# Performance work log

Measured on AMD Instinct MI355X. Metric: run time of the kernel, lower is better.

The kernel has to match this reference:

```python
import jax, jax.numpy as jnp
import numpy as np

N, E_SC, E_BB = 50000, 600000, 100000
D, ED, REMB, NRES, SBF = 128, 128, 32, 21, 16
PI = 3.14159


def ln(x, g, b):
    m = jnp.mean(x, -1, keepdims=True)
    v = jnp.mean((x - m) ** 2, -1, keepdims=True)
    return (x - m) * jax.lax.rsqrt(v + 1e-5) * g + b


def gcn(x, W, b, src, dst, w):
    # GCNConv: symmetric normalization with unit self-loops and edge weights w.
    n = x.shape[0]
    xw = x @ W
    deg = jax.ops.segment_sum(w, dst, num_segments=n) + 1.0  # +1 self-loop
    dis = jax.lax.rsqrt(jnp.maximum(deg, 1e-6))  # clamp: hat_e.mean can be negative
    norm = dis[src] * w * dis[dst]
    agg = jax.ops.segment_sum(norm[:, None] * xw[src], dst, num_segments=n)
    return agg + (dis * dis)[:, None] * xw + b


def core(V_com, SBF_chi, X_c_alpha, V_c_beta, SBF_phi, SBF_psi, d_sidechain_com, d_min,
         old_chi, old_phi, old_psi, old_cbeta_coords, old_calpha_coords,
         res_table, sc_ln_g, sc_ln_b, sc_W, sc_b, bb_ln_g, bb_ln_b, bb_W, bb_b,
         e_ln_g, e_ln_b, eW1, eb1, eW2, eb2, euW, eub, gW, gb, bgW, bgb,
         iW1, ib1, iW2, ib2, aW, ab, baW, bab, cW, cb, xW, xb,
         residue_idx_i, residue_idx_j, edge_index_sc, edge_index_bb):
    hat_h = ln(jnp.concatenate([V_com, SBF_chi], -1), sc_ln_g, sc_ln_b) @ sc_W + sc_b
    h = ln(jnp.concatenate([X_c_alpha, V_c_beta, SBF_phi, SBF_psi], -1), bb_ln_g, bb_ln_b) @ bb_W + bb_b
    pair = jnp.concatenate([res_table[residue_idx_i], res_table[residue_idx_j]], -1)
    e_in = jnp.concatenate([d_sidechain_com[:, None], d_min[:, None], pair], -1)
    hat_e = jax.nn.relu(ln(e_in, e_ln_g, e_ln_b) @ eW1 + eb1) @ eW2 + eb2
    src, dst = edge_index_sc[0], edge_index_sc[1]
    for _ in range(3):  # num_sidechain_layers
        w = hat_e.mean(-1)
        hat_h = hat_h + jax.nn.relu(gcn(hat_h, gW, gb, src, dst, w))
        hat_e = hat_e + jnp.concatenate([hat_h[src], hat_h[dst]], -1) @ euW + eub
    bsrc, bdst = edge_index_bb[0], edge_index_bb[1]
    ebb = jnp.ones(bsrc.shape[0], hat_h.dtype)
    for _ in range(2):
        m = jax.nn.relu(jnp.concatenate([h, hat_h], -1) @ iW1 + ib1) @ iW2 + ib2
        h = h + jax.nn.relu(gcn(h, bgW, bgb, bsrc, bdst, ebb)) + m
    sc_act = jax.nn.relu(hat_h)
    bb_act = jax.nn.relu(h)
    wrap = lambda a: (a + PI) % (2.0 * PI) - PI
    dchi = (sc_act @ aW + ab)[:, 0]
    chi_new = wrap(old_chi + dchi[None, :])  # [4, N]
    dphi = (bb_act @ baW + bab)[:, 0]
    phi_new = wrap(old_phi + dphi)
    psi_new = wrap(old_psi + dphi)  # same bb_angle_head applied twice in source
    V_cbeta_new = old_cbeta_coords + sc_act @ cW + cb
    X_calpha_new = old_calpha_coords + bb_act @ xW + xb
    return chi_new, phi_new, psi_new, V_cbeta_new, X_calpha_new


def setup_inputs() -> dict:
    key = jax.random.key(0)
    ks = jax.random.split(key, 40)
    rn = lambda i, s: jax.random.normal(ks[i], s, jnp.float32)
    p = lambda i, s: rn(i, s) * 0.05
    return dict(
        V_com=rn(0, (N, 3)), SBF_chi=rn(1, (N, SBF)), X_c_alpha=rn(2, (N, 3)),
        V_c_beta=rn(3, (N, 3)), SBF_phi=rn(4, (N, SBF)), SBF_psi=rn(5, (N, SBF)),
        d_sidechain_com=jax.random.uniform(ks[6], (E_SC,), jnp.float32),
        d_min=jax.random.uniform(ks[7], (E_SC,), jnp.float32),
        old_chi=rn(8, (4, N)), old_phi=rn(9, (N,)), old_psi=rn(10, (N,)),
        old_cbeta_coords=rn(11, (N, 3)), old_calpha_coords=rn(12, (N, 3)),
        res_table=p(13, (NRES, REMB)),
        sc_ln_g=jnp.ones(3 + SBF), sc_ln_b=jnp.zeros(3 + SBF), sc_W=p(14, (3 + SBF, D)), sc_b=jnp.zeros(D),
        bb_ln_g=jnp.ones(6 + 2 * SBF), bb_ln_b=jnp.zeros(6 + 2 * SBF), bb_W=p(15, (6 + 2 * SBF, D)), bb_b=jnp.zeros(D),
        e_ln_g=jnp.ones(2 + 2 * REMB), e_ln_b=jnp.zeros(2 + 2 * REMB),
        eW1=p(16, (2 + 2 * REMB, ED)), eb1=jnp.zeros(ED), eW2=p(17, (ED, ED)), eb2=jnp.zeros(ED),
        euW=p(18, (2 * D, ED)), eub=jnp.zeros(ED),
        gW=p(19, (D, D)), gb=jnp.zeros(D), bgW=p(20, (D, D)), bgb=jnp.zeros(D),
        iW1=p(21, (2 * D, D)), ib1=jnp.zeros(D), iW2=p(22, (D, D)), ib2=jnp.zeros(D),
        aW=p(23, (D, 1)), ab=jnp.zeros(1), baW=p(24, (D, 1)), bab=jnp.zeros(1),
        cW=p(25, (D, 3)), cb=jnp.zeros(3), xW=p(26, (D, 3)), xb=jnp.zeros(3),
        residue_idx_i=jax.random.randint(ks[27], (E_SC,), 0, NRES),
        residue_idx_j=jax.random.randint(ks[28], (E_SC,), 0, NRES),
        edge_index_sc=jax.random.randint(ks[29], (2, E_SC), 0, N),
        edge_index_bb=jax.random.randint(ks[30], (2, E_BB), 0, N),
    )


def reference(V_com, SBF_chi, X_c_alpha, V_c_beta, SBF_phi, SBF_psi, d_sidechain_com, d_min,
              old_chi, old_phi, old_psi, old_cbeta_coords, old_calpha_coords,
              res_table, sc_ln_g, sc_ln_b, sc_W, sc_b, bb_ln_g, bb_ln_b, bb_W, bb_b,
              e_ln_g, e_ln_b, eW1, eb1, eW2, eb2, euW, eub, gW, gb, bgW, bgb,
              iW1, ib1, iW2, ib2, aW, ab, baW, bab, cW, cb, xW, xb,
              residue_idx_i, residue_idx_j, edge_index_sc, edge_index_bb):
    return core(V_com, SBF_chi, X_c_alpha, V_c_beta, SBF_phi, SBF_psi, d_sidechain_com, d_min,
                old_chi, old_phi, old_psi, old_cbeta_coords, old_calpha_coords,
                res_table, sc_ln_g, sc_ln_b, sc_W, sc_b, bb_ln_g, bb_ln_b, bb_W, bb_b,
                e_ln_g, e_ln_b, eW1, eb1, eW2, eb2, euW, eub, gW, gb, bgW, bgb,
                iW1, ib1, iW2, ib2, aW, ab, baW, bab, cW, cb, xW, xb,
                residue_idx_i, residue_idx_j, edge_index_sc, edge_index_bb)
```

## Files before the change

### kernel.cpp

```cpp
#include <hip/hip_runtime.h>
#include <stdint.h>

#define DEVI __device__ __forceinline__

constexpr int N_   = 50000;
constexpr int ESC  = 600000;
constexpr int EBB  = 100000;
constexpr int NRES = 21;
constexpr float PI_F = 3.14159f;

constexpr int RCH = 2048;
constexpr int RBS = (ESC + RCH - 1)/RCH;
constexpr int RBB = (EBB + RCH - 1)/RCH;

typedef __attribute__((ext_vector_type(8))) short short8v;
typedef __attribute__((ext_vector_type(4))) float f32x4;

DEVI float bf2f(unsigned short u){ return __uint_as_float(((unsigned)u)<<16); }
DEVI unsigned short f2bf(float f){
  unsigned x = __float_as_uint(f);
  unsigned r = (x + 0x7FFFu + ((x>>16)&1u))>>16;
  return (unsigned short)r;
}
DEVI float ldin(const void* p, long i, int f32){
  return f32 ? ((const float*)p)[i] : bf2f(((const unsigned short*)p)[i]);
}
DEVI void stout(void* p, long i, float v, int f32){
  if(f32) ((float*)p)[i]=v; else ((unsigned short*)p)[i]=f2bf(v);
}
DEVI float wrapf(float a){
  float t = a + PI_F;
  const float TP = 2.f*PI_F;
  t -= floorf(t/TP)*TP;
  return t - PI_F;
}

constexpr int OW_SC_LN_G=0;
constexpr int OW_SC_LN_B=OW_SC_LN_G+19;
constexpr int OW_SC_W  = OW_SC_LN_B+19;
constexpr int OW_SC_B  = OW_SC_W+19*128;
constexpr int OW_BB_LN_G=OW_SC_B+128;
constexpr int OW_BB_LN_B=OW_BB_LN_G+38;
constexpr int OW_BB_W = OW_BB_LN_B+38;
constexpr int OW_BB_B = OW_BB_W+38*128;
constexpr int OW_E_LN_G=OW_BB_B+128;
constexpr int OW_E_LN_B=OW_E_LN_G+66;
constexpr int OW_EW1 = OW_E_LN_B+66;
constexpr int OW_EB1 = OW_EW1+66*128;
constexpr int OW_GW  = OW_EB1+128;
constexpr int OW_GB  = OW_GW+128*128;
constexpr int OW_BGW = OW_GB+128;
constexpr int OW_BGB = OW_BGW+128*128;
constexpr int OW_IW1 = OW_BGB+128;
constexpr int OW_IB1 = OW_IW1+256*128;
constexpr int OW_IW2 = OW_IB1+128;
constexpr int OW_IB2 = OW_IW2+128*128;
constexpr int OW_AW  = OW_IB2+128;
constexpr int OW_AB  = OW_AW+128;
constexpr int OW_BAW = OW_AB+1;
constexpr int OW_BAB = OW_BAW+128;
constexpr int OW_CW  = OW_BAB+1;
constexpr int OW_CB  = OW_CW+128*3;
constexpr int OW_XW  = OW_CB+3;
constexpr int OW_XB  = OW_XW+128*3;
constexpr int OW_RES = OW_XB+3;
constexpr int OW_TOT = OW_RES+21*32;

__global__ void k_detect(const void* vcom, int* flag){
  const unsigned short* u = (const unsigned short*)vcom;
  int insane=0;
  for(int i=0;i<64;i+=2){
    float f = bf2f(u[i]);
    float a = fabsf(f);
    if(!(a<1e5f) || (a!=0.0f && a<1e-5f)) insane++;
  }
  *flag = (insane>=8)?1:0;
}

struct CvtArgs { const void* src[29]; };

__global__ void k_cvtw(CvtArgs a, const int* flag, float* w){
  static constexpr int offs[30] = {
    OW_SC_LN_G,OW_SC_LN_B,OW_SC_W,OW_SC_B,OW_BB_LN_G,OW_BB_LN_B,OW_BB_W,OW_BB_B,
    OW_E_LN_G,OW_E_LN_B,OW_EW1,OW_EB1,OW_GW,OW_GB,OW_BGW,OW_BGB,OW_IW1,OW_IB1,
    OW_IW2,OW_IB2,OW_AW,OW_AB,OW_BAW,OW_BAB,OW_CW,OW_CB,OW_XW,OW_XB,OW_RES,OW_TOT};
  int f32=*flag;
  for(int t=blockIdx.x*blockDim.x+threadIdx.x; t<OW_TOT; t+=gridDim.x*blockDim.x){
    int s=0;
    while(t>=offs[s+1]) s++;
    w[t]=ldin(a.src[s], t-offs[s], f32);
  }
}

DEVI void wprep_pad(const float* W, int Kreal, unsigned short* hi, unsigned short* lo, int idx){
  int lane=idx&63, nt=(idx>>6)&7, kt=idx>>9;
  int n = nt*16 + (lane&15);
  int kbase = kt*32 + (lane>>4)*8;
  #pragma unroll
  for(int i=0;i<8;i++){
    int k=kbase+i;
    float v = (k<Kreal) ? W[(long)k*128 + n] : 0.f;
    unsigned short h = f2bf(v);
    hi[(long)idx*8+i]=h;
    if(lo){ float r = v - bf2f(h); lo[(long)idx*8+i]=f2bf(r); }
  }
}

constexpr int PB_WP = 46;
constexpr int PB_PV = PB_WP+1;
constexpr int PB_PP = PB_PV+441;
constexpr int PB_LN = PB_PP + (2*N_+3)/4;

__global__ void k_prep(const float* w, const int* flag,
    unsigned short* g_hi, unsigned short* g_lo,
    unsigned short* bg_hi,
    unsigned short* i2_hi,
    unsigned short* i1_hi,
    unsigned short* sc_hi, unsigned short* sc_lo,
    unsigned short* bb_hi, unsigned short* bb_lo,
    const void* eW2, const void* eb2, const void* euW, const void* eub,
    float* dv, float* dv4, float* P, float* sp, float* qp,
    const void* vcom, const void* sbfchi,
    const void* xca, const void* vcb, const void* sphi, const void* spsi,
    float* xn_sc, float* xn_bb){
  __shared__ float pv[64];
  int b=blockIdx.x;
  if(b<PB_WP){
    int idx=b*256+threadIdx.x;
    if(idx<2048)       wprep_pad(w+OW_GW,  128, g_hi,  g_lo,  idx);
    else if(idx<4096)  wprep_pad(w+OW_BGW, 128, bg_hi, nullptr, idx-2048);
    else if(idx<6144)  wprep_pad(w+OW_IW2, 128, i2_hi, nullptr, idx-4096);
    else if(idx<10240) wprep_pad(w+OW_IW1, 256, i1_hi, nullptr, idx-6144);
    else if(idx<10752) wprep_pad(w+OW_SC_W, 19, sc_hi, sc_lo, idx-10240);
    else if(idx<11776) wprep_pad(w+OW_BB_W, 38, bb_hi, bb_lo, idx-10752);
  } else if(b<PB_PV){
    int j=threadIdx.x; int f32=*flag;
    if(j<128){
      const float* g=w+OW_E_LN_G; const float* bb=w+OW_E_LN_B; const float* W1=w+OW_EW1;
      float A=g[0]*W1[j], C=g[1]*W1[128+j];
      float G=0,B=0;
      for(int i=0;i<66;i++){ float wij=W1[i*128+j]; G+=g[i]*wij; B+=bb[i]*wij; }
      B += w[OW_EB1+j];
      float v2=0; for(int k=0;k<128;k++) v2+=ldin(eW2,(long)j*128+k,f32);
      float us=0,ud=0;
      for(int k=0;k<128;k++){ us+=ldin(euW,(long)j*128+k,f32); ud+=ldin(euW,(long)(128+j)*128+k,f32); }
      dv[640+j]=us*(1.f/128.f); dv[768+j]=ud*(1.f/128.f);
      int j4=j>>2, r=j&3;
      dv4[j4*20+0+r]=A; dv4[j4*20+4+r]=C; dv4[j4*20+8+r]=G; dv4[j4*20+12+r]=B;
      dv4[j4*20+16+r]=v2*(1.f/128.f);
      if(j==0){
        float s=0,t=0;
        for(int k=0;k<128;k++){ s+=ldin(eb2,k,f32); t+=ldin(eub,k,f32); }
        dv[896]=s*(1.f/128.f); dv[897]=t*(1.f/128.f);
        dv4[640]=s*(1.f/128.f);
      }
    }
  } else if(b<PB_PP){
    int c=b-PB_PV, j=threadIdx.x;
    const float* res=w+OW_RES;
    if(j<32) pv[j]=res[(c/NRES)*32+j];
    else if(j<64) pv[j]=res[(c%NRES)*32+(j-32)];
    __syncthreads();
    if(j<128){
      const float* g=w+OW_E_LN_G; const float* W1=w+OW_EW1;
      float s=0;
      for(int i=0;i<64;i++) s += pv[i]*g[2+i]*W1[(2+i)*128+j];
      P[c*128+j]=s;
      if(j==0){ float a=0,q=0; for(int i=0;i<64;i++){a+=pv[i]; q+=pv[i]*pv[i];} sp[c]=a; qp[c]=q; }
    }
  } else {
    int wv=threadIdx.x>>6, lane=threadIdx.x&63;
    long gw=(long)(b-PB_PP)*4+wv;
    int f32=*flag;
    if(gw<N_){
      int n=(int)gw;
      float x=0.f;
      if(lane<3) x=ldin(vcom,(long)n*3+lane,f32);
      else if(lane<19) x=ldin(sbfchi,(long)n*16+(lane-3),f32);
      float s=x, q=x*x;
      for(int m=1;m<64;m<<=1){ s+=__shfl_xor(s,m,64); q+=__shfl_xor(q,m,64); }
      float mean=s*(1.f/19.f);
      float istd=rsqrtf(fmaxf(q*(1.f/19.f)-mean*mean,0.f)+1e-5f);
      if(lane<32){
        float xn=(lane<19)? (x-mean)*istd*w[OW_SC_LN_G+lane]+w[OW_SC_LN_B+lane] : 0.f;
        xn_sc[(long)n*32+lane]=xn;
      }
    } else if(gw<2L*N_){
      int n=(int)(gw-N_);
      float x=0.f;
      if(lane<3) x=ldin(xca,(long)n*3+lane,f32);
      else if(lane<6) x=ldin(vcb,(long)n*3+(lane-3),f32);
      else if(lane<22) x=ldin(sphi,(long)n*16+(lane-6),f32);
      else if(lane<38) x=ldin(spsi,(long)n*16+(lane-22),f32);
      float s=x, q=x*x;
      for(int m=1;m<64;m<<=1){ s+=__shfl_xor(s,m,64); q+=__shfl_xor(q,m,64); }
      float mean=s*(1.f/38.f);
      float istd=rsqrtf(fmaxf(q*(1.f/38.f)-mean*mean,0.f)+1e-5f);
      float xn=(lane<38)? (x-mean)*istd*w[OW_BB_LN_G+lane]+w[OW_BB_LN_B+lane] : 0.f;
      xn_bb[(long)n*64+lane]=xn;
    }
  }
}

__global__ void k_rhist(const int* key_sc, const int* key_bb, int shift, int* hist){
  __shared__ int h[256];
  h[threadIdx.x]=0; __syncthreads();
  int g = blockIdx.x>=RBS;
  const int* key = g? key_bb : key_sc;
  int E = g? EBB : ESC;
  int b = g? blockIdx.x-RBS : blockIdx.x;
  int base=b*RCH;
  for(int r=0;r<RCH/256;r++){
    int idx=base+r*256+threadIdx.x;
    if(idx<E) atomicAdd(&h[(key[idx]>>shift)&255],1);
  }
  __syncthreads();
  hist[(long)blockIdx.x*256+threadIdx.x]=h[threadIdx.x];
}
__global__ void k_rscanA(int* hist, int* tot){
  __shared__ int sA[512], sB[512];
  int g = blockIdx.x>=256;
  int d = blockIdx.x&255;
  int NB = g? RBB : RBS;
  int* H = hist + (g? (long)RBS*256 : 0);
  int t=threadIdx.x;
  int i0=t, i1=t+256;
  int o0 = (i0<NB)? H[(long)i0*256+d] : 0;
  int o1 = (i1<NB)? H[(long)i1*256+d] : 0;
  sA[i0]=o0; sA[i1]=o1;
  __syncthreads();
  int* a=sA; int* b=sB;
  for(int off=1; off<512; off<<=1){
    b[i0] = a[i0] + ((i0>=off)? a[i0-off]:0);
    b[i1] = a[i1] + ((i1>=off)? a[i1-off]:0);
    __syncthreads();
    int* tmp=a; a=b; b=tmp;
  }
  if(i0<NB) H[(long)i0*256+d] = a[i0]-o0;
  if(i1<NB) H[(long)i1*256+d] = a[i1]-o1;
  if(t==255) tot[(g?256:0)+d] = a[511];
}
__global__ void k_rscanB(const int* tot, int* base){
  __shared__ int sA[256], sB[256];
  int t=threadIdx.x;
  for(int g=0;g<2;g++){
    int o=tot[g*256+t];
    sA[t]=o; __syncthreads();
    int* a=sA; int* b=sB;
    for(int off=1; off<256; off<<=1){
      b[t] = a[t] + ((t>=off)? a[t-off]:0);
      __syncthreads();
      int* tmp=a; a=b; b=tmp;
    }
    base[g*256+t] = a[t]-o;
    __syncthreads();
  }
}
__global__ void k_rscat(int shift, int first,
    const int* kin_sc, const int* srcv_sc, const int2* pin_sc,
    const int* kin_bb, const int* srcv_bb, const int2* pin_bb,
    const int* hist, const int* dbase,
    int* kout_sc, int2* pout_sc, int* kout_bb, int2* pout_bb){
  __shared__ int running[256];
  __shared__ int Hb[256];
  __shared__ int whist[4][256];
  __shared__ int pw[4][256];
  int tid=threadIdx.x, lane=tid&63, w=tid>>6;
  int g = blockIdx.x>=RBS;
  const int* kin  = g? kin_bb : kin_sc;
  const int* srcv = g? srcv_bb: srcv_sc;
  const int2* pin = g? pin_bb : pin_sc;
  int* kout  = g? kout_bb : kout_sc;
  int2* pout = g? pout_bb : pout_sc;
  int E = g? EBB : ESC;
  int b = g? blockIdx.x-RBS : blockIdx.x;
  running[tid]=0;
  Hb[tid]=hist[(long)blockIdx.x*256+tid] + dbase[(g?256:0)+tid];
  int base=b*RCH;
  for(int r=0;r<RCH/256;r++){
    __syncthreads();
    whist[0][tid]=0; whist[1][tid]=0; whist[2][tid]=0; whist[3][tid]=0;
    __syncthreads();
    int idx=base+r*256+tid;
    bool valid = idx<E;
    int key=0, digit=0; int2 pay; pay.x=0; pay.y=0;
    if(valid){
      key=kin[idx];
      digit=(key>>shift)&255;
      if(first){ pay.x=srcv[idx]; pay.y=idx; }
      else pay=pin[idx];
    }
    unsigned long long act=__ballot(valid);
    unsigned long long same=act;
    #pragma unroll
    for(int k=0;k<8;k++){
      unsigned long long m=__ballot(valid && ((digit>>k)&1));
      same &= ((digit>>k)&1)? m : ~m;
    }
    same &= act;
    unsigned long long below=(1ULL<<lane)-1ULL;
    int wrank=__popcll(same & below);
    if(valid && wrank==0) whist[w][digit]=__popcll(same);
    __syncthreads();
    int c0=whist[0][tid], c1=whist[1][tid], c2=whist[2][tid], c3=whist[3][tid];
    pw[0][tid]=0; pw[1][tid]=c0; pw[2][tid]=c0+c1; pw[3][tid]=c0+c1+c2;
    __syncthreads();
    if(valid){
      int pos=Hb[digit]+running[digit]+pw[w][digit]+wrank;
      kout[pos]=key; pout[pos]=pay;
    }
    __syncthreads();
    running[tid]+=c0+c1+c2+c3;
  }
}
__global__ void k_bounds(const int* dstS_sc, const int* dstS_bb, int* rp_sc, int* rp_bb){
  long i=(long)blockIdx.x*blockDim.x+threadIdx.x;
  if(i<=ESC){
    int cur = (i<ESC)? dstS_sc[i] : N_;
    int prev= (i>0)? dstS_sc[i-1] : -1;
    for(int d=prev+1; d<=cur; d++) rp_sc[d]=(int)i;
  } else if(i <= (long)ESC+1+EBB){
    long j=i-(ESC+1);
    int cur = (j<EBB)? dstS_bb[j] : N_;
    int prev= (j>0)? dstS_bb[j-1] : -1;
    for(int d=prev+1; d<=cur; d++) rp_bb[d]=(int)j;
  }
}
__global__ void k_degb(const int* rp, float* disb){
  int n=blockIdx.x*blockDim.x+threadIdx.x;
  if(n<N_) disb[n]=rsqrtf(1.f+(float)(rp[n+1]-rp[n]));
}

constexpr int WB4 = (ESC + 1023)/1024;
__global__ __launch_bounds__(256,4) void k_w0(const void* dsc, const void* dmin,
    const int* ri_, const int* rj_, const int* flag, const float* dv4,
    const float* P, const float* sp, const float* qp, float* we){
  long base=(long)blockIdx.x*1024+threadIdx.x;
  int f32=*flag;
  float d1[4],d2[4],istd[4],nmi[4],acc[4];
  int cc[4]; bool val[4];
  #pragma unroll
  for(int k=0;k<4;k++){
    long e=base+k*256;
    val[k]= e<ESC;
    long ee= val[k]? e : 0;
    d1[k]=ldin(dsc,ee,f32); d2[k]=ldin(dmin,ee,f32);
    int c=ri_[ee]*NRES+rj_[ee];
    cc[k]=c;
    float m=(d1[k]+d2[k]+sp[c])*(1.f/66.f);
    float ms=(d1[k]*d1[k]+d2[k]*d2[k]+qp[c])*(1.f/66.f);
    istd[k]=rsqrtf(fmaxf(ms-m*m,0.f)+1e-5f);
    nmi[k]=-m*istd[k];
    acc[k]=0.f;
  }
  #pragma unroll 2
  for(int j4=0;j4<32;j4++){
    const float4* q=(const float4*)&dv4[j4*20];
    float4 A4=q[0], C4=q[1], G4=q[2], B4=q[3], V4=q[4];
    #pragma unroll
    for(int k=0;k<4;k++){
      float4 P4=*(const float4*)&P[(long)cc[k]*128+j4*4];
      float t,hid;
      t=fmaf(d1[k],A4.x,fmaf(d2[k],C4.x,P4.x)); hid=fmaf(istd[k],t,fmaf(nmi[k],G4.x,B4.x)); acc[k]=fmaf(fmaxf(hid,0.f),V4.x,acc[k]);
      t=fmaf(d1[k],A4.y,fmaf(d2[k],C4.y,P4.y)); hid=fmaf(istd[k],t,fmaf(nmi[k],G4.y,B4.y)); acc[k]=fmaf(fmaxf(hid,0.f),V4.y,acc[k]);
      t=fmaf(d1[k],A4.z,fmaf(d2[k],C4.z,P4.z)); hid=fmaf(istd[k],t,fmaf(nmi[k],G4.z,B4.z)); acc[k]=fmaf(fmaxf(hid,0.f),V4.z,acc[k]);
      t=fmaf(d1[k],A4.w,fmaf(d2[k],C4.w,P4.w)); hid=fmaf(istd[k],t,fmaf(nmi[k],G4.w,B4.w)); acc[k]=fmaf(fmaxf(hid,0.f),V4.w,acc[k]);
    }
  }
  float e2=dv4[640];
  #pragma unroll
  for(int k=0;k<4;k++) if(val[k]) we[base+k*256]=acc[k]+e2;
}

__global__ void k_deg(const int* rp, const int2* se, const float* we_edge,
                      const float* an, const float* bn, const float* dv,
                      float* we_csr, float* dis, int layer){
  int n=blockIdx.x*blockDim.x+threadIdx.x;
  if(n>=N_) return;
  int e0=rp[n], e1=rp[n+1];
  float s=1.f;
  if(layer==0){
    for(int p=e0;p<e1;p++){ float ww=we_edge[se[p].y]; we_csr[p]=ww; s+=ww; }
  } else {
    float add_n = bn[n] + dv[897];
    for(int p=e0;p<e1;p++){
      float ww=we_csr[p] + an[se[p].x] + add_n;
      we_csr[p]=ww; s+=ww;
    }
  }
  dis[n]=rsqrtf(fmaxf(s,1e-6f));
}
__global__ void k_norm(const int2* se, const float* we_csr, const float* dis, float* wn){
  int p=blockIdx.x*blockDim.x+threadIdx.x;
  if(p<ESC) wn[p]=dis[se[p].x]*we_csr[p];
}

DEVI f32x4 MFMA(short8v a, short8v b, f32x4 c){
  return __builtin_amdgcn_mfma_f32_16x16x32_bf16(a,b,c,0,0,0);
}
DEVI void cvt8(float4 a0, float4 a1, short8v& hi, short8v& lo){
  float av[8]={a0.x,a0.y,a0.z,a0.w,a1.x,a1.y,a1.z,a1.w};
  union{short8v v; unsigned short u[8];} H,L;
  #pragma unroll
  for(int i=0;i<8;i++){
    unsigned short h=f2bf(av[i]);
    float r=av[i]-bf2f(h);
    H.u[i]=h; L.u[i]=f2bf(r);
  }
  hi=H.v; lo=L.v;
}
DEVI short8v cvt8hi(float4 a0, float4 a1){
  union{short8v v; unsigned short u[8];} H;
  H.u[0]=f2bf(a0.x); H.u[1]=f2bf(a0.y); H.u[2]=f2bf(a0.z); H.u[3]=f2bf(a0.w);
  H.u[4]=f2bf(a1.x); H.u[5]=f2bf(a1.y); H.u[6]=f2bf(a1.z); H.u[7]=f2bf(a1.w);
  return H.v;
}

template<int KT, int LDA>
DEVI void mgemm_body(int bid, const float* A1, const float* A2,
    const unsigned short* Whi, const unsigned short* Wlo,
    const float* bias, float* C, int relu, int accum, int M){
  const int lane = threadIdx.x & 63;
  const int wid  = threadIdx.x >> 6;
  const int r0   = bid*64 + wid*16;
  const int mrow = lane & 15;
  const int kg   = lane >> 4;
  long arow = (long)min(r0 + mrow, M-1);
  f32x4 acc[8];
  #pragma unroll
  for(int t=0;t<8;t++) acc[t]=(f32x4){0.f,0.f,0.f,0.f};

  #pragma unroll
  for(int kt=0; kt<KT; kt++){
    const float* A = (KT==8 && kt>=4) ? A2 : A1;
    int kb = (kt&3)*32 + kg*8;
    float4 a0 = *(const float4*)&A[arow*LDA + kb];
    float4 a1 = *(const float4*)&A[arow*LDA + kb + 4];
    short8v ah, al; cvt8(a0,a1,ah,al);
    #pragma unroll
    for(int nt=0;nt<8;nt++){
      long off = (((long)kt*8+nt)*64 + lane)*8;
      short8v wh = *(const short8v*)&Whi[off];
      short8v wl = *(const short8v*)&Wlo[off];
      acc[nt] = MFMA(ah, wh, acc[nt]);
      acc[nt] = MFMA(al, wh, acc[nt]);
      acc[nt] = MFMA(ah, wl, acc[nt]);
      acc[nt] = MFMA(al, wl, acc[nt]);
    }
  }

  #pragma unroll
  for(int nt=0;nt<8;nt++){
    int col = nt*16 + mrow;
    float bj = bias ? bias[col] : 0.f;
    #pragma unroll
    for(int r=0;r<4;r++){
      int row = r0 + kg*4 + r;
      if(row >= M) continue;
      long idx = (long)row*128 + col;
      float v = acc[nt][r] + bj;
      if(relu) v = fmaxf(v,0.f);
      if(accum) v += C[idx];
      C[idx] = v;
    }
  }
}

template<int KT, int LDA>
__global__ __launch_bounds__(256,4) void k_mgemm(const float* A1, const float* A2,
    const unsigned short* Whi, const unsigned short* Wlo,
    const float* bias, float* C, int relu, int accum, int M){
  mgemm_body<KT,LDA>(blockIdx.x, A1, A2, Whi, Wlo, bias, C, relu, accum, M);
}

__global__ __launch_bounds__(256,4) void k_mfeat(const float* xn_sc, const float* xn_bb,
    const unsigned short* schi, const unsigned short* sclo,
    const unsigned short* bbhi, const unsigned short* bblo,
    const float* w, float* hat_h, float* hbuf, int M){
  int GBl=(M+63)/64;
  if((int)blockIdx.x < GBl)
    mgemm_body<1,32>(blockIdx.x, xn_sc, nullptr, schi, sclo, w+OW_SC_B, hat_h, 0,0,M);
  else
    mgemm_body<2,64>(blockIdx.x-GBl, xn_bb, nullptr, bbhi, bblo, w+OW_BB_B, hbuf, 0,0,M);
}

__global__ __launch_bounds__(256,4) void k_mbb(const float* h, const float* hh,
    const unsigned short* W1hi,
    const unsigned short* W2hi,
    const unsigned short* W3hi,
    const float* b1, const float* b2,
    float* xwout, float* mout, int M){
  __shared__ unsigned short hids[64*136];
  const int lane = threadIdx.x & 63;
  const int wid  = threadIdx.x >> 6;
  const int r0   = blockIdx.x*64 + wid*16;
  const int mrow = lane & 15;
  const int kg   = lane >> 4;
  long arow = (long)min(r0 + mrow, M-1);
  f32x4 acc1[8], acc2[8];
  #pragma unroll
  for(int t=0;t<8;t++){ acc1[t]=(f32x4){0,0,0,0}; acc2[t]=(f32x4){0,0,0,0}; }

  #pragma unroll
  for(int kt=0; kt<8; kt++){
    const float* A = (kt>=4) ? hh : h;
    int kb = (kt&3)*32 + kg*8;
    float4 a0 = *(const float4*)&A[arow*128 + kb];
    float4 a1 = *(const float4*)&A[arow*128 + kb + 4];
    short8v ah = cvt8hi(a0,a1);
    #pragma unroll
    for(int nt=0;nt<8;nt++){
      long off = (((long)kt*8+nt)*64 + lane)*8;
      acc1[nt] = MFMA(ah, *(const short8v*)&W1hi[off], acc1[nt]);
    }
    if(kt<4){
      #pragma unroll
      for(int nt=0;nt<8;nt++){
        long off = (((long)kt*8+nt)*64 + lane)*8;
        acc2[nt] = MFMA(ah, *(const short8v*)&W2hi[off], acc2[nt]);
      }
    }
  }

  #pragma unroll
  for(int nt=0;nt<8;nt++){
    int col = nt*16 + mrow;
    float bj = b1[col];
    #pragma unroll
    for(int r=0;r<4;r++){
      int rloc = wid*16 + kg*4 + r;
      int row = r0 + kg*4 + r;
      hids[rloc*136 + col] = f2bf(fmaxf(acc1[nt][r] + bj, 0.f));
      if(row < M) xwout[(long)row*128 + col] = acc2[nt][r];
    }
  }
  __syncthreads();

  f32x4 acc3[8];
  #pragma unroll
  for(int t=0;t<8;t++) acc3[t]=(f32x4){0,0,0,0};
  int rloc = wid*16 + mrow;
  #pragma unroll
  for(int kt=0; kt<4; kt++){
    int kb = kt*32 + kg*8;
    short8v ah = *(const short8v*)&hids[rloc*136 + kb];
    #pragma unroll
    for(int nt=0;nt<8;nt++){
      long off = (((long)kt*8+nt)*64 + lane)*8;
      acc3[nt] = MFMA(ah, *(const short8v*)&W3hi[off], acc3[nt]);
    }
  }
  #pragma unroll
  for(int nt=0;nt<8;nt++){
    int col = nt*16 + mrow;
    float bj = b2[col];
    #pragma unroll
    for(int r=0;r<4;r++){
      int row = r0 + kg*4 + r;
      if(row < M) mout[(long)row*128 + col] = acc3[nt][r] + bj;
    }
  }
}

__global__ void k_agg_sc(const int* rp, const int2* se, const float* wn,
                         const float* dis, const float* xw, const float* w,
                         float* hat_h, const float* dv, float* an, float* bn, int withdot){
  int wv=threadIdx.x>>6, lane=threadIdx.x&63;
  int n=blockIdx.x*4+wv;
  int g=lane>>4, l=lane&15, d0=l*8;
  float disn=dis[n];
  float4 aA={0,0,0,0}, aB={0,0,0,0};
  int e0=rp[n], e1=rp[n+1];
  for(int p=e0+g; p<e1; p+=4){
    int s0=se[p].x;
    float nw=wn[p];
    float4 xa=*(const float4*)&xw[(long)s0*128+d0];
    float4 xb=*(const float4*)&xw[(long)s0*128+d0+4];
    aA.x+=nw*xa.x; aA.y+=nw*xa.y; aA.z+=nw*xa.z; aA.w+=nw*xa.w;
    aB.x+=nw*xb.x; aB.y+=nw*xb.y; aB.z+=nw*xb.z; aB.w+=nw*xb.w;
  }
  #pragma unroll
  for(int m=16;m<64;m<<=1){
    aA.x+=__shfl_xor(aA.x,m,64); aA.y+=__shfl_xor(aA.y,m,64);
    aA.z+=__shfl_xor(aA.z,m,64); aA.w+=__shfl_xor(aA.w,m,64);
    aB.x+=__shfl_xor(aB.x,m,64); aB.y+=__shfl_xor(aB.y,m,64);
    aB.z+=__shfl_xor(aB.z,m,64); aB.w+=__shfl_xor(aB.w,m,64);
  }
  float d2=disn*disn;
  float4 xsA=*(const float4*)&xw[(long)n*128+d0];
  float4 xsB=*(const float4*)&xw[(long)n*128+d0+4];
  float4 gbA=*(const float4*)&w[OW_GB+d0];
  float4 gbB=*(const float4*)&w[OW_GB+d0+4];
  float4 hoA=*(const float4*)&hat_h[(long)n*128+d0];
  float4 hoB=*(const float4*)&hat_h[(long)n*128+d0+4];
  float4 hA, hB;
  hA.x=hoA.x+fmaxf(aA.x*disn+d2*xsA.x+gbA.x,0.f);
  hA.y=hoA.y+fmaxf(aA.y*disn+d2*xsA.y+gbA.y,0.f);
  hA.z=hoA.z+fmaxf(aA.z*disn+d2*xsA.z+gbA.z,0.f);
  hA.w=hoA.w+fmaxf(aA.w*disn+d2*xsA.w+gbA.w,0.f);
  hB.x=hoB.x+fmaxf(aB.x*disn+d2*xsB.x+gbB.x,0.f);
  hB.y=hoB.y+fmaxf(aB.y*disn+d2*xsB.y+gbB.y,0.f);
  hB.z=hoB.z+fmaxf(aB.z*disn+d2*xsB.z+gbB.z,0.f);
  hB.w=hoB.w+fmaxf(aB.w*disn+d2*xsB.w+gbB.w,0.f);
  if(g==0){
    *(float4*)&hat_h[(long)n*128+d0]=hA;
    *(float4*)&hat_h[(long)n*128+d0+4]=hB;
  }
  if(withdot){
    float4 usA=*(const float4*)&dv[640+d0], usB=*(const float4*)&dv[640+d0+4];
    float4 udA=*(const float4*)&dv[768+d0], udB=*(const float4*)&dv[768+d0+4];
    float a = hA.x*usA.x+hA.y*usA.y+hA.z*usA.z+hA.w*usA.w
            + hB.x*usB.x+hB.y*usB.y+hB.z*usB.z+hB.w*usB.w;
    float b = hA.x*udA.x+hA.y*udA.y+hA.z*udA.z+hA.w*udA.w
            + hB.x*udB.x+hB.y*udB.y+hB.z*udB.z+hB.w*udB.w;
    #pragma unroll
    for(int m=1;m<16;m<<=1){ a+=__shfl_xor(a,m,64); b+=__shfl_xor(b,m,64); }
    if(lane==0){ an[n]=a; bn[n]=b; }
  }
}

__global__ void k_agg_bb(const int* rp, const int2* se, const float* disb,
                         const float* xw, const float* mbuf, const float* w, float* h){
  int wv=threadIdx.x>>6, lane=threadIdx.x&63;
  int n=blockIdx.x*4+wv;
  int g=lane>>4, l=lane&15, d0=l*8;
  int e0=rp[n], e1=rp[n+1];
  float disn=disb[n];
  float4 aA={0,0,0,0}, aB={0,0,0,0};
  for(int p=e0+g; p<e1; p+=4){
    int s0=se[p].x;
    float nw=disb[s0];
    float4 xa=*(const float4*)&xw[(long)s0*128+d0];
    float4 xb=*(const float4*)&xw[(long)s0*128+d0+4];
    aA.x+=nw*xa.x; aA.y+=nw*xa.y; aA.z+=nw*xa.z; aA.w+=nw*xa.w;
    aB.x+=nw*xb.x; aB.y+=nw*xb.y; aB.z+=nw*xb.z; aB.w+=nw*xb.w;
  }
  #pragma unroll
  for(int m=16;m<64;m<<=1){
    aA.x+=__shfl_xor(aA.x,m,64); aA.y+=__shfl_xor(aA.y,m,64);
    aA.z+=__shfl_xor(aA.z,m,64); aA.w+=__shfl_xor(aA.w,m,64);
    aB.x+=__shfl_xor(aB.x,m,64); aB.y+=__shfl_xor(aB.y,m,64);
    aB.z+=__shfl_xor(aB.z,m,64); aB.w+=__shfl_xor(aB.w,m,64);
  }
  if(g==0){
    float d2=disn*disn;
    float4 xsA=*(const float4*)&xw[(long)n*128+d0];
    float4 xsB=*(const float4*)&xw[(long)n*128+d0+4];
    float4 gbA=*(const float4*)&w[OW_BGB+d0];
    float4 gbB=*(const float4*)&w[OW_BGB+d0+4];
    float4 mA=*(const float4*)&mbuf[(long)n*128+d0];
    float4 mB=*(const float4*)&mbuf[(long)n*128+d0+4];
    float4 hA=*(float4*)&h[(long)n*128+d0];
    float4 hB=*(float4*)&h[(long)n*128+d0+4];
    hA.x+=fmaxf(aA.x*disn+d2*xsA.x+gbA.x,0.f)+mA.x;
    hA.y+=fmaxf(aA.y*disn+d2*xsA.y+gbA.y,0.f)+mA.y;
    hA.z+=fmaxf(aA.z*disn+d2*xsA.z+gbA.z,0.f)+mA.z;
    hA.w+=fmaxf(aA.w*disn+d2*xsA.w+gbA.w,0.f)+mA.w;
    hB.x+=fmaxf(aB.x*disn+d2*xsB.x+gbB.x,0.f)+mB.x;
    hB.y+=fmaxf(aB.y*disn+d2*xsB.y+gbB.y,0.f)+mB.y;
    hB.z+=fmaxf(aB.z*disn+d2*xsB.z+gbB.z,0.f)+mB.z;
    hB.w+=fmaxf(aB.w*disn+d2*xsB.w+gbB.w,0.f)+mB.w;
    *(float4*)&h[(long)n*128+d0]=hA;
    *(float4*)&h[(long)n*128+d0+4]=hB;
  }
}

__global__ void k_heads(const float* hat_h, const float* h, const float* w,
                        const void* old_chi, const void* old_phi, const void* old_psi,
                        const void* old_cb, const void* old_ca, const int* flag, void* out){
  int wv=threadIdx.x>>6, lane=threadIdx.x&63;
  int n=blockIdx.x*4+wv;
  int f32=*flag;
  float s0=fmaxf(hat_h[(long)n*128+lane],0.f), s1=fmaxf(hat_h[(long)n*128+64+lane],0.f);
  float b0=fmaxf(h[(long)n*128+lane],0.f),    b1=fmaxf(h[(long)n*128+64+lane],0.f);
  float r[8];
  r[0]=s0*w[OW_AW+lane]+s1*w[OW_AW+64+lane];
  r[1]=s0*w[OW_CW+lane*3+0]+s1*w[OW_CW+(64+lane)*3+0];
  r[2]=s0*w[OW_CW+lane*3+1]+s1*w[OW_CW+(64+lane)*3+1];
  r[3]=s0*w[OW_CW+lane*3+2]+s1*w[OW_CW+(64+lane)*3+2];
  r[4]=b0*w[OW_BAW+lane]+b1*w[OW_BAW+64+lane];
  r[5]=b0*w[OW_XW+lane*3+0]+b1*w[OW_XW+(64+lane)*3+0];
  r[6]=b0*w[OW_XW+lane*3+1]+b1*w[OW_XW+(64+lane)*3+1];
  r[7]=b0*w[OW_XW+lane*3+2]+b1*w[OW_XW+(64+lane)*3+2];
  for(int m=1;m<64;m<<=1){
    #pragma unroll
    for(int t=0;t<8;t++) r[t]+=__shfl_xor(r[t],m,64);
  }
  if(lane==0){
    float dchi=r[0]+w[OW_AB];
    for(int k=0;k<4;k++)
      stout(out,(long)k*N_+n, wrapf(ldin(old_chi,(long)k*N_+n,f32)+dchi), f32);
    float dphi=r[4]+w[OW_BAB];
    stout(out,(long)4*N_+n, wrapf(ldin(old_phi,n,f32)+dphi), f32);
    stout(out,(long)5*N_+n, wrapf(ldin(old_psi,n,f32)+dphi), f32);
    for(int t=0;t<3;t++){
      stout(out,(long)6*N_+(long)n*3+t, ldin(old_cb,(long)n*3+t,f32)+r[1+t]+w[OW_CB+t], f32);
      stout(out,(long)9*N_+(long)n*3+t, ldin(old_ca,(long)n*3+t,f32)+r[5+t]+w[OW_XB+t], f32);
    }
  }
}

extern "C" void kernel_launch(void* const* d_in, const int* in_sizes, int n_in,
                              void* d_out, int out_size, void* d_ws, size_t ws_size,
                              hipStream_t stream) {
  (void)in_sizes; (void)n_in; (void)out_size; (void)ws_size;

  char* p=(char*)d_ws;
  auto alloc=[&](size_t bytes)->void*{ void* r=(void*)p; p+=((bytes+255)&~(size_t)255); return r; };
  int*   flag   =(int*)  alloc(16);
  float* warena =(float*)alloc((size_t)OW_TOT*4);
  float* dv     =(float*)alloc(1024*4);
  float* dv4    =(float*)alloc(1024*4);
  float* P      =(float*)alloc((size_t)441*128*4);
  float* sp     =(float*)alloc(441*4);
  float* qp     =(float*)alloc(441*4);
  float* hat_h  =(float*)alloc((size_t)N_*128*4);
  float* hbuf   =(float*)alloc((size_t)N_*128*4);
  float* bufX   =(float*)alloc((size_t)N_*128*4);
  float* bufM   =(float*)alloc((size_t)N_*128*4);
  float* xn_sc  =(float*)alloc((size_t)N_*32*4);
  float* xn_bb  =(float*)alloc((size_t)N_*64*4);
  float* we     =(float*)alloc((size_t)ESC*4);
  float* we_csr =(float*)alloc((size_t)ESC*4);
  float* wn     =(float*)alloc((size_t)ESC*4);
  float* an     =(float*)alloc((size_t)N_*4);
  float* bn     =(float*)alloc((size_t)N_*4);
  float* dis    =(float*)alloc((size_t)N_*4);
  float* disb   =(float*)alloc((size_t)N_*4);
  int* rp_sc    =(int*)  alloc((size_t)(N_+1)*4);
  int* rp_bb    =(int*)  alloc((size_t)(N_+1)*4);
  int*  key1_sc =(int*)  alloc((size_t)ESC*4);
  int2* pay1_sc =(int2*) alloc((size_t)ESC*8);
  int*  dstS_sc =(int*)  alloc((size_t)ESC*4);
  int2* csr_se_sc=(int2*)alloc((size_t)ESC*8);
  int*  key1_bb =(int*)  alloc((size_t)EBB*4);
  int2* pay1_bb =(int2*) alloc((size_t)EBB*8);
  int*  dstS_bb =(int*)  alloc((size_t)EBB*4);
  int2* csr_se_bb=(int2*)alloc((size_t)EBB*8);
  int*  hist    =(int*)  alloc((size_t)(RBS+RBB)*256*4);
  int*  tot     =(int*)  alloc(512*4);
  int*  dbase   =(int*)  alloc(512*4);
  unsigned short* wfg_hi =(unsigned short*)alloc(2048*8*2);
  unsigned short* wfg_lo =(unsigned short*)alloc(2048*8*2);
  unsigned short* wfbg_hi=(unsigned short*)alloc(2048*8*2);
  unsigned short* wfi2_hi=(unsigned short*)alloc(2048*8*2);
  unsigned short* wfi1_hi=(unsigned short*)alloc(4096*8*2);
  unsigned short* wfsc_hi=(unsigned short*)alloc(512*8*2);
  unsigned short* wfsc_lo=(unsigned short*)alloc(512*8*2);
  unsigned short* wfbb_hi=(unsigned short*)alloc(1024*8*2);
  unsigned short* wfbb_lo=(unsigned short*)alloc(1024*8*2);

  const int* src_sc=(const int*)d_in[48];
  const int* dst_sc=src_sc+ESC;
  const int* src_bb=(const int*)d_in[49];
  const int* dst_bb=src_bb+EBB;

  k_detect<<<1,1,0,stream>>>(d_in[0], flag);

  CvtArgs ca;
  {
    int map[29]={14,15,16,17,18,19,20,21,22,23,24,25,30,31,32,33,34,35,36,37,
                 38,39,40,41,42,43,44,45,13};
    for(int i=0;i<29;i++) ca.src[i]=d_in[map[i]];
  }
  k_cvtw<<<(OW_TOT+255)/256,256,0,stream>>>(ca, flag, warena);

  k_prep<<<PB_LN,256,0,stream>>>(warena, flag,
      wfg_hi,wfg_lo, wfbg_hi, wfi2_hi, wfi1_hi,
      wfsc_hi,wfsc_lo, wfbb_hi,wfbb_lo,
      d_in[26], d_in[27], d_in[28], d_in[29], dv, dv4, P, sp, qp,
      d_in[0], d_in[1], d_in[2], d_in[3], d_in[4], d_in[5], xn_sc, xn_bb);

  k_rhist<<<RBS+RBB,256,0,stream>>>(dst_sc, dst_bb, 0, hist);
  k_rscanA<<<512,256,0,stream>>>(hist, tot);
  k_rscanB<<<1,256,0,stream>>>(tot, dbase);
  k_rscat<<<RBS+RBB,256,0,stream>>>(0, 1, dst_sc, src_sc, (const int2*)nullptr,
                                    dst_bb, src_bb, (const int2*)nullptr, hist, dbase,
                                    key1_sc, pay1_sc, key1_bb, pay1_bb);
  k_rhist<<<RBS+RBB,256,0,stream>>>(key1_sc, key1_bb, 8, hist);
  k_rscanA<<<512,256,0,stream>>>(hist, tot);
  k_rscanB<<<1,256,0,stream>>>(tot, dbase);
  k_rscat<<<RBS+RBB,256,0,stream>>>(8, 0, key1_sc, (const int*)nullptr, pay1_sc,
                                    key1_bb, (const int*)nullptr, pay1_bb, hist, dbase,
                                    dstS_sc, csr_se_sc, dstS_bb, csr_se_bb);
  k_bounds<<<(int)(((long)ESC+1+EBB+1+255)/256),256,0,stream>>>(dstS_sc, dstS_bb, rp_sc, rp_bb);
  k_degb<<<(N_+255)/256,256,0,stream>>>(rp_bb, disb);

  const int GB = (N_+63)/64;
  k_mfeat<<<2*GB,256,0,stream>>>(xn_sc, xn_bb, wfsc_hi, wfsc_lo, wfbb_hi, wfbb_lo,
                                 warena, hat_h, hbuf, N_);

  k_w0<<<WB4,256,0,stream>>>(d_in[6],d_in[7],(const int*)d_in[46],(const int*)d_in[47],
                             flag,dv4,P,sp,qp,we);

  const int DB = (N_+255)/256;
  const int NB = (ESC+255)/256;
  for(int l=0;l<3;l++){
    k_deg<<<DB,256,0,stream>>>(rp_sc, csr_se_sc, we, an, bn, dv, we_csr, dis, l);
    k_norm<<<NB,256,0,stream>>>(csr_se_sc, we_csr, dis, wn);
    k_mgemm<4,128><<<GB,256,0,stream>>>(hat_h, nullptr, wfg_hi, wfg_lo, nullptr, bufX, 0, 0, N_);
    k_agg_sc<<<N_/4,256,0,stream>>>(rp_sc,csr_se_sc,wn,dis,bufX,warena,hat_h,dv,an,bn,(l<2)?1:0);
  }

  for(int l=0;l<2;l++){
    k_mbb<<<GB,256,0,stream>>>(hbuf, hat_h, wfi1_hi, wfbg_hi, wfi2_hi,
                               warena+OW_IB1, warena+OW_IB2, bufX, bufM, N_);
    k_agg_bb<<<N_/4,256,0,stream>>>(rp_bb,csr_se_bb,disb,bufX,bufM,warena,hbuf);
  }

  k_heads<<<N_/4,256,0,stream>>>(hat_h,hbuf,warena,
                                 d_in[8],d_in[9],d_in[10],d_in[11],d_in[12],flag,d_out);
}
```

Before: 639.6 us.

## Split edge-weight hidden dimension across 16 lanes with shuffle reduction in k_w0

The initial edge-weight kernel moves from one thread per edge (four edges per thread, looping over all 128 hidden units) to sixteen lanes per edge, each covering eight hidden units, combined with an xor-shuffle reduction. The per-unit coefficient table changes from interleaved float4 groups to five flat 128-wide arrays so each lane loads contiguous slices. This aims to cut per-thread serial ALU work and raise occupancy. In exchange it launches far more threads, repeats the per-edge layer-norm statistics and index loads in every lane, and adds shuffle overhead.

```diff
diff --git a/kernel.cpp b/kernel.cpp
--- a/kernel.cpp
+++ b/kernel.cpp
@@ -119,7 +119,7 @@
     unsigned short* sc_hi, unsigned short* sc_lo,
     unsigned short* bb_hi, unsigned short* bb_lo,
     const void* eW2, const void* eb2, const void* euW, const void* eub,
-    float* dv, float* dv4, float* P, float* sp, float* qp,
+    float* dv, float* dvf, float* P, float* sp, float* qp,
     const void* vcom, const void* sbfchi,
     const void* xca, const void* vcb, const void* sphi, const void* spsi,
     float* xn_sc, float* xn_bb){
@@ -145,14 +145,12 @@
       float us=0,ud=0;
       for(int k=0;k<128;k++){ us+=ldin(euW,(long)j*128+k,f32); ud+=ldin(euW,(long)(128+j)*128+k,f32); }
       dv[640+j]=us*(1.f/128.f); dv[768+j]=ud*(1.f/128.f);
-      int j4=j>>2, r=j&3;
-      dv4[j4*20+0+r]=A; dv4[j4*20+4+r]=C; dv4[j4*20+8+r]=G; dv4[j4*20+12+r]=B;
-      dv4[j4*20+16+r]=v2*(1.f/128.f);
+      dvf[j]=A; dvf[128+j]=C; dvf[256+j]=G; dvf[384+j]=B; dvf[512+j]=v2*(1.f/128.f);
       if(j==0){
         float s=0,t=0;
         for(int k=0;k<128;k++){ s+=ldin(eb2,k,f32); t+=ldin(eub,k,f32); }
         dv[896]=s*(1.f/128.f); dv[897]=t*(1.f/128.f);
-        dv4[640]=s*(1.f/128.f);
+        dvf[640]=s*(1.f/128.f);
       }
     }
   } else if(b<PB_PP){
@@ -331,45 +329,41 @@
   if(n<N_) disb[n]=rsqrtf(1.f+(float)(rp[n+1]-rp[n]));
 }
 
-constexpr int WB4 = (ESC + 1023)/1024;
-__global__ __launch_bounds__(256,4) void k_w0(const void* dsc, const void* dmin,
-    const int* ri_, const int* rj_, const int* flag, const float* dv4,
+constexpr int WBE = (ESC + 15)/16;
+__global__ __launch_bounds__(256,8) void k_w0(const void* dsc, const void* dmin,
+    const int* ri_, const int* rj_, const int* flag, const float* dvf,
     const float* P, const float* sp, const float* qp, float* we){
-  long base=(long)blockIdx.x*1024+threadIdx.x;
+  int wv=threadIdx.x>>6, lane=threadIdx.x&63;
+  int g=lane>>4, l=lane&15;
+  long e=(long)blockIdx.x*16 + wv*4 + g;
+  bool val = e<ESC;
+  long ee = val? e : 0;
   int f32=*flag;
-  float d1[4],d2[4],istd[4],nmi[4],acc[4];
-  int cc[4]; bool val[4];
-  #pragma unroll
-  for(int k=0;k<4;k++){
-    long e=base+k*256;
-    val[k]= e<ESC;
-    long ee= val[k]? e : 0;
-    d1[k]=ldin(dsc,ee,f32); d2[k]=ldin(dmin,ee,f32);
-    int c=ri_[ee]*NRES+rj_[ee];
-    cc[k]=c;
-    float m=(d1[k]+d2[k]+sp[c])*(1.f/66.f);
-    float ms=(d1[k]*d1[k]+d2[k]*d2[k]+qp[c])*(1.f/66.f);
-    istd[k]=rsqrtf(fmaxf(ms-m*m,0.f)+1e-5f);
-    nmi[k]=-m*istd[k];
-    acc[k]=0.f;
-  }
-  #pragma unroll 2
-  for(int j4=0;j4<32;j4++){
-    const float4* q=(const float4*)&dv4[j4*20];
-    float4 A4=q[0], C4=q[1], G4=q[2], B4=q[3], V4=q[4];
-    #pragma unroll
-    for(int k=0;k<4;k++){
-      float4 P4=*(const float4*)&P[(long)cc[k]*128+j4*4];
-      float t,hid;
-      t=fmaf(d1[k],A4.x,fmaf(d2[k],C4.x,P4.x)); hid=fmaf(istd[k],t,fmaf(nmi[k],G4.x,B4.x)); acc[k]=fmaf(fmaxf(hid,0.f),V4.x,acc[k]);
-      t=fmaf(d1[k],A4.y,fmaf(d2[k],C4.y,P4.y)); hid=fmaf(istd[k],t,fmaf(nmi[k],G4.y,B4.y)); acc[k]=fmaf(fmaxf(hid,0.f),V4.y,acc[k]);
-      t=fmaf(d1[k],A4.z,fmaf(d2[k],C4.z,P4.z)); hid=fmaf(istd[k],t,fmaf(nmi[k],G4.z,B4.z)); acc[k]=fmaf(fmaxf(hid,0.f),V4.z,acc[k]);
-      t=fmaf(d1[k],A4.w,fmaf(d2[k],C4.w,P4.w)); hid=fmaf(istd[k],t,fmaf(nmi[k],G4.w,B4.w)); acc[k]=fmaf(fmaxf(hid,0.f),V4.w,acc[k]);
-    }
-  }
-  float e2=dv4[640];
-  #pragma unroll
-  for(int k=0;k<4;k++) if(val[k]) we[base+k*256]=acc[k]+e2;
+  float d1=ldin(dsc,ee,f32), d2=ldin(dmin,ee,f32);
+  int c=ri_[ee]*NRES+rj_[ee];
+  float m=(d1+d2+sp[c])*(1.f/66.f);
+  float ms=(d1*d1+d2*d2+qp[c])*(1.f/66.f);
+  float istd=rsqrtf(fmaxf(ms-m*m,0.f)+1e-5f);
+  float nmi=-m*istd;
+  int j0=l*8;
+  float4 A0=*(const float4*)&dvf[j0],     A1=*(const float4*)&dvf[j0+4];
+  float4 C0=*(const float4*)&dvf[128+j0], C1=*(const float4*)&dvf[128+j0+4];
+  float4 G0=*(const float4*)&dvf[256+j0], G1=*(const float4*)&dvf[256+j0+4];
+  float4 B0=*(const float4*)&dvf[384+j0], B1=*(const float4*)&dvf[384+j0+4];
+  float4 V0=*(const float4*)&dvf[512+j0], V1=*(const float4*)&dvf[512+j0+4];
+  float4 P0=*(const float4*)&P[(long)c*128+j0], P1=*(const float4*)&P[(long)c*128+j0+4];
+  float acc=0.f, t, hid;
+  t=fmaf(d1,A0.x,fmaf(d2,C0.x,P0.x)); hid=fmaf(istd,t,fmaf(nmi,G0.x,B0.x)); acc=fmaf(fmaxf(hid,0.f),V0.x,acc);
+  t=fmaf(d1,A0.y,fmaf(d2,C0.y,P0.y)); hid=fmaf(istd,t,fmaf(nmi,G0.y,B0.y)); acc=fmaf(fmaxf(hid,0.f),V0.y,acc);
+  t=fmaf(d1,A0.z,fmaf(d2,C0.z,P0.z)); hid=fmaf(istd,t,fmaf(nmi,G0.z,B0.z)); acc=fmaf(fmaxf(hid,0.f),V0.z,acc);
+  t=fmaf(d1,A0.w,fmaf(d2,C0.w,P0.w)); hid=fmaf(istd,t,fmaf(nmi,G0.w,B0.w)); acc=fmaf(fmaxf(hid,0.f),V0.w,acc);
+  t=fmaf(d1,A1.x,fmaf(d2,C1.x,P1.x)); hid=fmaf(istd,t,fmaf(nmi,G1.x,B1.x)); acc=fmaf(fmaxf(hid,0.f),V1.x,acc);
+  t=fmaf(d1,A1.y,fmaf(d2,C1.y,P1.y)); hid=fmaf(istd,t,fmaf(nmi,G1.y,B1.y)); acc=fmaf(fmaxf(hid,0.f),V1.y,acc);
+  t=fmaf(d1,A1.z,fmaf(d2,C1.z,P1.z)); hid=fmaf(istd,t,fmaf(nmi,G1.z,B1.z)); acc=fmaf(fmaxf(hid,0.f),V1.z,acc);
+  t=fmaf(d1,A1.w,fmaf(d2,C1.w,P1.w)); hid=fmaf(istd,t,fmaf(nmi,G1.w,B1.w)); acc=fmaf(fmaxf(hid,0.f),V1.w,acc);
+  #pragma unroll
+  for(int msk=1;msk<16;msk<<=1) acc+=__shfl_xor(acc,msk,64);
+  if(l==0 && val) we[e]=acc+dvf[640];
 }
 
 __global__ void k_deg(const int* rp, const int2* se, const float* we_edge,
@@ -710,7 +704,7 @@
   int*   flag   =(int*)  alloc(16);
   float* warena =(float*)alloc((size_t)OW_TOT*4);
   float* dv     =(float*)alloc(1024*4);
-  float* dv4    =(float*)alloc(1024*4);
+  float* dvf    =(float*)alloc(1024*4);
   float* P      =(float*)alloc((size_t)441*128*4);
   float* sp     =(float*)alloc(441*4);
   float* qp     =(float*)alloc(441*4);
@@ -768,7 +762,7 @@
   k_prep<<<PB_LN,256,0,stream>>>(warena, flag,
       wfg_hi,wfg_lo, wfbg_hi, wfi2_hi, wfi1_hi,
       wfsc_hi,wfsc_lo, wfbb_hi,wfbb_lo,
-      d_in[26], d_in[27], d_in[28], d_in[29], dv, dv4, P, sp, qp,
+      d_in[26], d_in[27], d_in[28], d_in[29], dv, dvf, P, sp, qp,
       d_in[0], d_in[1], d_in[2], d_in[3], d_in[4], d_in[5], xn_sc, xn_bb);
 
   k_rhist<<<RBS+RBB,256,0,stream>>>(dst_sc, dst_bb, 0, hist);
@@ -790,8 +784,8 @@
   k_mfeat<<<2*GB,256,0,stream>>>(xn_sc, xn_bb, wfsc_hi, wfsc_lo, wfbb_hi, wfbb_lo,
                                  warena, hat_h, hbuf, N_);
 
-  k_w0<<<WB4,256,0,stream>>>(d_in[6],d_in[7],(const int*)d_in[46],(const int*)d_in[47],
-                             flag,dv4,P,sp,qp,we);
+  k_w0<<<WBE,256,0,stream>>>(d_in[6],d_in[7],(const int*)d_in[46],(const int*)d_in[47],
+                             flag,dvf,P,sp,qp,we);
 
   const int DB = (N_+255)/256;
   const int NB = (ESC+255)/256;
```

After: 649.6 us. About the same (+1.6%).
